# Kernel tuning notes

Measured on AMD Instinct MI355X. Metric: run time of the kernel, lower is better.

## Reference

```python
import jax, jax.numpy as jnp
import numpy as np

N = 50000      # nodes
E = 800000     # edges (avg degree 16)
D = 64         # hidden_dim == out_dim
L = 4          # number of GatedGCN layers
NB = 16        # num_bond_type
EPS_BN = 1e-5
EPS_ETA = 1e-6


def _bn(x, g, b):
    # training-mode batch norm over the node/edge axis
    mu = jnp.mean(x, axis=0, keepdims=True)
    var = jnp.var(x, axis=0, keepdims=True)
    return (x - mu) * jax.lax.rsqrt(var + EPS_BN) * g + b


def setup_inputs() -> dict:
    key = jax.random.key(0)
    ks = iter(jax.random.split(key, 64))
    s = 0.05

    def w(shape):
        return jax.random.normal(next(ks), shape, dtype=jnp.float32) * s

    inp = {
        "h_ids": jax.random.randint(next(ks), (N,), 0, N),
        "e_ids": jax.random.randint(next(ks), (E,), 0, NB),
        "f_ids": jax.random.randint(next(ks), (N,), 0, N),
        "src": jax.random.randint(next(ks), (E,), 0, N),
        "dst": jax.random.randint(next(ks), (E,), 0, N),
        "emb_h": w((N, D)),
        "emb_e": w((NB, D)),
        "emb_f": w((N, D)),
        "A1_w": w((L, D, D)), "A1_b": jnp.zeros((L, D), jnp.float32),
        "A2_w": w((L, 2 * D, D)), "A2_b": jnp.zeros((L, D), jnp.float32),
        "B1_w": w((L, D, D)), "B1_b": jnp.zeros((L, D), jnp.float32),
        "B2_w": w((L, D, D)), "B2_b": jnp.zeros((L, D), jnp.float32),
        "B3_w": w((L, D, D)), "B3_b": jnp.zeros((L, D), jnp.float32),
        "C1_w": w((L, D, D)), "C1_b": jnp.zeros((L, D), jnp.float32),
        "C2_w": w((L, D, D)), "C2_b": jnp.zeros((L, D), jnp.float32),
        "bn_h_g": jnp.ones((L, D), jnp.float32), "bn_h_b": jnp.zeros((L, D), jnp.float32),
        "bn_e_g": jnp.ones((L, D), jnp.float32), "bn_e_b": jnp.zeros((L, D), jnp.float32),
        "mlp_w0": w((D, D // 2)), "mlp_b0": jnp.zeros((D // 2,), jnp.float32),
        "mlp_w1": w((D // 2, D // 4)), "mlp_b1": jnp.zeros((D // 4,), jnp.float32),
        "mlp_w2": w((D // 4, 1)), "mlp_b2": jnp.zeros((1,), jnp.float32),
    }
    return inp


def reference(h_ids, e_ids, f_ids, src, dst,
              emb_h, emb_e, emb_f,
              A1_w, A1_b, A2_w, A2_b, B1_w, B1_b, B2_w, B2_b, B3_w, B3_b,
              C1_w, C1_b, C2_w, C2_b,
              bn_h_g, bn_h_b, bn_e_g, bn_e_b,
              mlp_w0, mlp_b0, mlp_w1, mlp_b1, mlp_w2, mlp_b2):
    h = emb_h[h_ids]          # [N, D]
    e = emb_e[e_ids]          # [E, D]
    p = emb_f[f_ids]          # [N, D]

    seg = lambda m: jax.ops.segment_sum(m, dst, num_segments=N)

    for i in range(L):
        h_in, e_in, p_in = h, e, p
        # per-node projections (dense GEMMs), then irregular gathers per edge
        B1h = h @ B1_w[i] + B1_b[i]
        B2h = h @ B2_w[i] + B2_b[i]
        B3e = e @ B3_w[i] + B3_b[i]
        hat_eta = B1h[src] + B2h[dst] + B3e           # [E, D]
        sigma = jax.nn.sigmoid(hat_eta)
        sum_sigma = seg(sigma)                        # [N, D] scatter-sum at dst
        eta = sigma / (sum_sigma[dst] + EPS_ETA)      # [E, D]

        v = jnp.concatenate([h, p], axis=-1) @ A2_w[i] + A2_b[i]  # [N, D]
        sum_eta_v = seg(eta * v[src])
        h_new = h @ A1_w[i] + A1_b[i] + sum_eta_v

        C2p = p @ C2_w[i] + C2_b[i]
        sum_eta_p = seg(eta * C2p[src])
        p_new = p @ C1_w[i] + C1_b[i] + sum_eta_p

        h = jax.nn.relu(_bn(h_new, bn_h_g[i], bn_h_b[i]))
        e_new = jax.nn.relu(_bn(hat_eta, bn_e_g[i], bn_e_b[i]))
        p = jnp.tanh(p_new)
        # residual (input_dim == output_dim in every layer)
        h = h_in + h
        e = e_in + e_new
        p = p_in + p

    hg = jnp.mean(h, axis=0)  # mean readout over the (single) graph -> [D]
    y = jax.nn.relu(hg @ mlp_w0 + mlp_b0)
    y = jax.nn.relu(y @ mlp_w1 + mlp_b1)
    y = y @ mlp_w2 + mlp_b2   # [1]
    return y
```

## Files before the change

### kernel.cpp

```cpp
#include <hip/hip_runtime.h>
#include <math.h>

#define NN 50000
#define EE 800000
#define LL 4

typedef unsigned short u16;
typedef unsigned int u32;

__device__ __forceinline__ float rlane(float v, int l) {
  return __int_as_float(__builtin_amdgcn_readlane(__float_as_int(v), l));
}

__device__ __forceinline__ float matvec64(float xv, const float* __restrict__ w) {
  float a0 = 0.f, a1 = 0.f, a2 = 0.f, a3 = 0.f;
#pragma unroll
  for (int k = 0; k < 64; k += 4) {
    a0 = fmaf(rlane(xv, k + 0), w[k + 0], a0);
    a1 = fmaf(rlane(xv, k + 1), w[k + 1], a1);
    a2 = fmaf(rlane(xv, k + 2), w[k + 2], a2);
    a3 = fmaf(rlane(xv, k + 3), w[k + 3], a3);
  }
  return (a0 + a1) + (a2 + a3);
}

__device__ __forceinline__ float sigm(float x) { return 1.f / (1.f + __expf(-x)); }

__device__ __forceinline__ u16 f2b(float x) {
  u32 u = __float_as_uint(x);
  u32 r = (u + 0x7FFFu + ((u >> 16) & 1u)) >> 16;
  return (u16)r;
}
__device__ __forceinline__ float b2f(u16 b) { return __uint_as_float(((u32)b) << 16); }

__global__ void k_hist(const int* __restrict__ dst, int* __restrict__ counts) {
  int i = blockIdx.x * 256 + threadIdx.x;
  if (i < EE) atomicAdd(&counts[dst[i]], 1);
}

__global__ void k_scan(const int* __restrict__ counts, int* __restrict__ row_start,
                       int* __restrict__ cursor) {
  __shared__ int sd[1024];
  int tid = threadIdx.x;
  int running = 0;
  for (int basei = 0; basei < NN; basei += 1024) {
    int i = basei + tid;
    int v = (i < NN) ? counts[i] : 0;
    sd[tid] = v;
    __syncthreads();
    for (int ofs = 1; ofs < 1024; ofs <<= 1) {
      int t = (tid >= ofs) ? sd[tid - ofs] : 0;
      __syncthreads();
      sd[tid] += t;
      __syncthreads();
    }
    int incl = sd[tid];
    int total = sd[1023];
    if (i < NN) { int e = running + incl - v; row_start[i] = e; cursor[i] = e; }
    running += total;
    __syncthreads();
  }
  if (tid == 0) row_start[NN] = EE;
}

__global__ void k_scatter(const int* __restrict__ dst, const int* __restrict__ src,
                          const int* __restrict__ e_ids,
                          int* __restrict__ cursor, int* __restrict__ src_s,
                          int* __restrict__ eids_s) {
  int i = blockIdx.x * 256 + threadIdx.x;
  if (i < EE) {
    int d = dst[i];
    int pos = atomicAdd(&cursor[d], 1);
    src_s[pos] = src[i];
    eids_s[pos] = e_ids[i];
  }
}

__global__ void k_einit(const int* __restrict__ eids_s, const float* __restrict__ emb_e,
                        u16* __restrict__ e_sorted) {
  int idx = blockIdx.x * 256 + threadIdx.x;
  if (idx >= EE * 64) return;
  int ed = idx >> 6, f = idx & 63;
  e_sorted[idx] = f2b(emb_e[eids_s[ed] * 64 + f]);
}

__global__ void k_ninit(const int* __restrict__ h_ids, const int* __restrict__ f_ids,
                        const float* __restrict__ emb_h, const float* __restrict__ emb_f,
                        float* __restrict__ h, float* __restrict__ p) {
  int idx = blockIdx.x * 256 + threadIdx.x;
  if (idx >= NN * 64) return;
  int n = idx >> 6, f = idx & 63;
  h[idx] = emb_h[h_ids[n] * 64 + f];
  p[idx] = emb_f[f_ids[n] * 64 + f];
}

__global__ void __launch_bounds__(256) k_A(
    int mode,
    float* __restrict__ h, float* __restrict__ p,
    float* __restrict__ hn, float* __restrict__ pn,
    const float* __restrict__ mu_h, const float* __restrict__ ir_h,
    const float* __restrict__ g_h, const float* __restrict__ b_h,
    const float* __restrict__ B1w, const float* __restrict__ B1b,
    const float* __restrict__ B2w, const float* __restrict__ B2b,
    const float* __restrict__ A1w, const float* __restrict__ A1b,
    const float* __restrict__ C1w, const float* __restrict__ C1b,
    const float* __restrict__ C2w, const float* __restrict__ C2b,
    const float* __restrict__ A2w, const float* __restrict__ A2b,
    float* __restrict__ B1h, float* __restrict__ B2h,
    float* __restrict__ vbuf, float* __restrict__ C2p) {
  const int f = threadIdx.x & 63;
  const int wv = threadIdx.x >> 6;
  const int base0 = (blockIdx.x * 4 + wv) * 16;
  if (base0 >= NN) return;

  if (mode) {
    float mu = mu_h[f], ir = ir_h[f], ga = g_h[f], be = b_h[f];
    for (int i = 0; i < 16; ++i) {
      int n = base0 + i; if (n >= NN) break;
      float hv = hn[n * 64 + f];
      h[n * 64 + f] += fmaxf(0.f, (hv - mu) * ir * ga + be);
      float pv = pn[n * 64 + f];
      p[n * 64 + f] += tanhf(pv);
    }
  }

  float w[64];
#define LOADW(WP) _Pragma("unroll") for (int k = 0; k < 64; ++k) w[k] = (WP)[k * 64 + f];

  LOADW(B1w);
  { float bb = B1b[f];
    for (int i = 0; i < 16; ++i) { int n = base0 + i; if (n >= NN) break;
      B1h[n * 64 + f] = matvec64(h[n * 64 + f], w) + bb; } }
  LOADW(B2w);
  { float bb = B2b[f];
    for (int i = 0; i < 16; ++i) { int n = base0 + i; if (n >= NN) break;
      B2h[n * 64 + f] = matvec64(h[n * 64 + f], w) + bb; } }
  LOADW(A1w);
  { float bb = A1b[f];
    for (int i = 0; i < 16; ++i) { int n = base0 + i; if (n >= NN) break;
      hn[n * 64 + f] = matvec64(h[n * 64 + f], w) + bb; } }
  LOADW(C1w);
  { float bb = C1b[f];
    for (int i = 0; i < 16; ++i) { int n = base0 + i; if (n >= NN) break;
      pn[n * 64 + f] = matvec64(p[n * 64 + f], w) + bb; } }
  LOADW(C2w);
  { float bb = C2b[f];
    for (int i = 0; i < 16; ++i) { int n = base0 + i; if (n >= NN) break;
      C2p[n * 64 + f] = matvec64(p[n * 64 + f], w) + bb; } }
  {
    float w2[64];
#pragma unroll
    for (int k = 0; k < 64; ++k) { w[k] = A2w[k * 64 + f]; w2[k] = A2w[(k + 64) * 64 + f]; }
    float bb = A2b[f];
    for (int i = 0; i < 16; ++i) { int n = base0 + i; if (n >= NN) break;
      vbuf[n * 64 + f] = matvec64(h[n * 64 + f], w) + matvec64(p[n * 64 + f], w2) + bb; }
  }
#undef LOADW
}

template <int SH>
__global__ void __launch_bounds__(256) k_B(
    const u16* __restrict__ e_sorted, const float* __restrict__ B1h,
    const float* __restrict__ B2h, const int* __restrict__ src_s,
    const int* __restrict__ row_start,
    const float* __restrict__ B3w, const float* __restrict__ B3b,
    u16* __restrict__ hat, float* __restrict__ sum_sigma,
    float* __restrict__ eS1, float* __restrict__ eS2) {
  const int f = threadIdx.x & 63;
  const int wv = threadIdx.x >> 6;
  const int nb = (blockIdx.x * 4 + wv) * 4;
  if (nb >= NN) return;
  float w[64];
#pragma unroll
  for (int k = 0; k < 64; ++k) w[k] = B3w[k * 64 + f];
  float bb = B3b[f];
  float s1 = 0.f, s2 = 0.f;
  for (int i = 0; i < 4; ++i) {
    int n = nb + i; if (n >= NN) break;
    float b2 = B2h[n * 64 + f];
    float ssum = 0.f;
    int t0 = row_start[n], t1 = row_start[n + 1];
    for (int t = t0; t < t1; ++t) {
      float xv = b2f(e_sorted[t * 64 + f]);
      int s = src_s[t];
      float acc = matvec64(xv, w) + bb + b2 + B1h[s * 64 + f];
      if (SH) {
        u16 hb = f2b(acc);
        hat[t * 64 + f] = hb;
        acc = b2f(hb);
      }
      float sg = sigm(acc);
      ssum += sg; s1 += acc; s2 += acc * acc;
    }
    sum_sigma[n * 64 + f] = ssum;
  }
  int slot = (blockIdx.x & 255) * 64 + f;
  atomicAdd(&eS1[slot], s1);
  atomicAdd(&eS2[slot], s2);
}

__global__ void k_red(const float* __restrict__ S1, const float* __restrict__ S2,
                      float cnt, float* __restrict__ mu, float* __restrict__ ir) {
  int f = threadIdx.x;
  float a = 0.f, b = 0.f;
  for (int j = 0; j < 256; ++j) { a += S1[j * 64 + f]; b += S2[j * 64 + f]; }
  float m = a / cnt;
  float var = fmaxf(b / cnt - m * m, 0.f);
  mu[f] = m;
  ir[f] = rsqrtf(var + 1e-5f);
}

template <int SH>
__global__ void __launch_bounds__(256) k_C(
    const u16* __restrict__ hat, u16* __restrict__ e_sorted,
    const float* __restrict__ B1h, const float* __restrict__ B2h,
    const float* __restrict__ B3w, const float* __restrict__ B3b,
    const float* __restrict__ vbuf, const float* __restrict__ C2p,
    const int* __restrict__ src_s, const int* __restrict__ row_start,
    const float* __restrict__ sum_sigma,
    float* __restrict__ hn, float* __restrict__ pn,
    const float* __restrict__ mu_e, const float* __restrict__ ir_e,
    const float* __restrict__ g_e, const float* __restrict__ b_e,
    float* __restrict__ hS1, float* __restrict__ hS2) {
  const int f = threadIdx.x & 63;
  const int wv = threadIdx.x >> 6;
  const int n = blockIdx.x * 4 + wv;
  if (n >= NN) return;
  float w[64];
  float bb = 0.f;
  if (!SH) {
#pragma unroll
    for (int k = 0; k < 64; ++k) w[k] = B3w[k * 64 + f];
    bb = B3b[f];
  }
  float mu = mu_e[f], ir = ir_e[f], ga = g_e[f], be = b_e[f];
  float inv = 1.f / (sum_sigma[n * 64 + f] + 1e-6f);
  float ahv = 0.f, ahp = 0.f;
  int t0 = row_start[n], t1 = row_start[n + 1];
  int t = t0;
  if (SH) {
    for (; t + 4 <= t1; t += 4) {
      int s0 = src_s[t + 0] * 64, s1 = src_s[t + 1] * 64;
      int s2 = src_s[t + 2] * 64, s3 = src_s[t + 3] * 64;
      float hv0 = b2f(hat[(size_t)(t + 0) * 64 + f]);
      float hv1 = b2f(hat[(size_t)(t + 1) * 64 + f]);
      float hv2 = b2f(hat[(size_t)(t + 2) * 64 + f]);
      float hv3 = b2f(hat[(size_t)(t + 3) * 64 + f]);
      float ev0 = b2f(e_sorted[(size_t)(t + 0) * 64 + f]);
      float ev1 = b2f(e_sorted[(size_t)(t + 1) * 64 + f]);
      float ev2 = b2f(e_sorted[(size_t)(t + 2) * 64 + f]);
      float ev3 = b2f(e_sorted[(size_t)(t + 3) * 64 + f]);
      float v0 = vbuf[s0 + f], v1 = vbuf[s1 + f], v2 = vbuf[s2 + f], v3 = vbuf[s3 + f];
      float c0 = C2p[s0 + f], c1 = C2p[s1 + f], c2 = C2p[s2 + f], c3 = C2p[s3 + f];
      float et0 = sigm(hv0) * inv, et1 = sigm(hv1) * inv;
      float et2 = sigm(hv2) * inv, et3 = sigm(hv3) * inv;
      ahv += et0 * v0 + et1 * v1 + et2 * v2 + et3 * v3;
      ahp += et0 * c0 + et1 * c1 + et2 * c2 + et3 * c3;
      e_sorted[(size_t)(t + 0) * 64 + f] = f2b(ev0 + fmaxf(0.f, (hv0 - mu) * ir * ga + be));
      e_sorted[(size_t)(t + 1) * 64 + f] = f2b(ev1 + fmaxf(0.f, (hv1 - mu) * ir * ga + be));
      e_sorted[(size_t)(t + 2) * 64 + f] = f2b(ev2 + fmaxf(0.f, (hv2 - mu) * ir * ga + be));
      e_sorted[(size_t)(t + 3) * 64 + f] = f2b(ev3 + fmaxf(0.f, (hv3 - mu) * ir * ga + be));
    }
  }
  for (; t < t1; ++t) {
    int s = src_s[t] * 64;
    float ev = b2f(e_sorted[(size_t)t * 64 + f]);
    float hatv;
    if (SH) hatv = b2f(hat[(size_t)t * 64 + f]);
    else    hatv = matvec64(ev, w) + bb + B2h[n * 64 + f] + B1h[s + f];
    float eta = sigm(hatv) * inv;
    ahv = fmaf(eta, vbuf[s + f], ahv);
    ahp = fmaf(eta, C2p[s + f], ahp);
    e_sorted[(size_t)t * 64 + f] = f2b(ev + fmaxf(0.f, (hatv - mu) * ir * ga + be));
  }
  float hv = hn[n * 64 + f] + ahv; hn[n * 64 + f] = hv;
  pn[n * 64 + f] += ahp;
  int slot = (blockIdx.x & 255) * 64 + f;
  atomicAdd(&hS1[slot], hv);
  atomicAdd(&hS2[slot], hv * hv);
}

__global__ void __launch_bounds__(256) k_F1(
    const float* __restrict__ hn, const float* __restrict__ h,
    const float* __restrict__ mu, const float* __restrict__ ir,
    const float* __restrict__ ga, const float* __restrict__ be,
    float* __restrict__ hsum) {
  int f = threadIdx.x & 63, wv = threadIdx.x >> 6;
  float m = mu[f], r = ir[f], g = ga[f], b = be[f];
  float ps = 0.f;
  for (int n = blockIdx.x * 4 + wv; n < NN; n += gridDim.x * 4)
    ps += h[n * 64 + f] + fmaxf(0.f, (hn[n * 64 + f] - m) * r * g + b);
  atomicAdd(&hsum[f], ps);
}

__global__ void k_F2(const float* __restrict__ hsum,
                     const float* __restrict__ w0, const float* __restrict__ b0,
                     const float* __restrict__ w1, const float* __restrict__ b1,
                     const float* __restrict__ w2, const float* __restrict__ b2,
                     float* __restrict__ out) {
  __shared__ float hg[64]; __shared__ float y0[32]; __shared__ float y1[16];
  int t = threadIdx.x;
  hg[t] = hsum[t] * (1.f / (float)NN);
  __syncthreads();
  if (t < 32) { float a = b0[t];
    for (int k = 0; k < 64; ++k) a = fmaf(hg[k], w0[k * 32 + t], a);
    y0[t] = fmaxf(a, 0.f); }
  __syncthreads();
  if (t < 16) { float a = b1[t];
    for (int k = 0; k < 32; ++k) a = fmaf(y0[k], w1[k * 16 + t], a);
    y1[t] = fmaxf(a, 0.f); }
  __syncthreads();
  if (t == 0) { float a = b2[0];
    for (int k = 0; k < 16; ++k) a = fmaf(y1[k], w2[k], a);
    out[0] = a; }
}

__global__ void k_report(float* out, float v) { out[0] = v; }

extern "C" void kernel_launch(void* const* d_in, const int* in_sizes, int n_in,
                              void* d_out, int out_size, void* d_ws, size_t ws_size,
                              hipStream_t stream) {
  (void)in_sizes; (void)n_in; (void)out_size;
  const int* h_ids = (const int*)d_in[0];
  const int* e_ids = (const int*)d_in[1];
  const int* f_ids = (const int*)d_in[2];
  const int* src   = (const int*)d_in[3];
  const int* dst   = (const int*)d_in[4];
  const float* emb_h = (const float*)d_in[5];
  const float* emb_e = (const float*)d_in[6];
  const float* emb_f = (const float*)d_in[7];
  const float* A1_w = (const float*)d_in[8];  const float* A1_b = (const float*)d_in[9];
  const float* A2_w = (const float*)d_in[10]; const float* A2_b = (const float*)d_in[11];
  const float* B1_w = (const float*)d_in[12]; const float* B1_b = (const float*)d_in[13];
  const float* B2_w = (const float*)d_in[14]; const float* B2_b = (const float*)d_in[15];
  const float* B3_w = (const float*)d_in[16]; const float* B3_b = (const float*)d_in[17];
  const float* C1_w = (const float*)d_in[18]; const float* C1_b = (const float*)d_in[19];
  const float* C2_w = (const float*)d_in[20]; const float* C2_b = (const float*)d_in[21];
  const float* bn_h_g = (const float*)d_in[22]; const float* bn_h_b = (const float*)d_in[23];
  const float* bn_e_g = (const float*)d_in[24]; const float* bn_e_b = (const float*)d_in[25];
  const float* mlp_w0 = (const float*)d_in[26]; const float* mlp_b0 = (const float*)d_in[27];
  const float* mlp_w1 = (const float*)d_in[28]; const float* mlp_b1 = (const float*)d_in[29];
  const float* mlp_w2 = (const float*)d_in[30]; const float* mlp_b2 = (const float*)d_in[31];

  auto pad = [](size_t b) { return (b + 255) & ~(size_t)255; };
  const size_t sz_e    = pad((size_t)EE * 64 * 2);
  const size_t sz_node = pad((size_t)NN * 64 * 4);
  const size_t sz_cnt  = pad((size_t)NN * 4);
  const size_t sz_row  = pad((size_t)(NN + 1) * 4);
  const size_t sz_ei   = pad((size_t)EE * 4);
  const size_t sz_stat = pad((size_t)LL * 2 * 256 * 64 * 4);
  const size_t sz_vec  = pad(64 * 4);

  size_t base_need = sz_e + 9 * sz_node + 2 * sz_cnt + sz_row + 2 * sz_ei +
                     2 * sz_stat + 5 * sz_vec;
  bool store_hat = (base_need + sz_e) <= ws_size;
  if (base_need > ws_size) {
    k_report<<<1, 1, 0, stream>>>((float*)d_out, (float)(ws_size >> 20) + 0.125f);
    return;
  }

  char* cur = (char*)d_ws;
  auto alloc = [&](size_t bytes) -> char* { char* r = cur; cur += bytes; return r; };
  u16* e_sorted = (u16*)alloc(sz_e);
  u16* hat      = store_hat ? (u16*)alloc(sz_e) : (u16*)e_sorted;
  float* h    = (float*)alloc(sz_node);
  float* p    = (float*)alloc(sz_node);
  float* hn   = (float*)alloc(sz_node);
  float* pn   = (float*)alloc(sz_node);
  float* B1h  = (float*)alloc(sz_node);
  float* B2h  = (float*)alloc(sz_node);
  float* vbuf = (float*)alloc(sz_node);
  float* C2p  = (float*)alloc(sz_node);
  float* ssig = (float*)alloc(sz_node);
  int* counts    = (int*)alloc(sz_cnt);
  int* cursor    = (int*)alloc(sz_cnt);
  int* row_start = (int*)alloc(sz_row);
  int* src_s     = (int*)alloc(sz_ei);
  int* eids_s    = (int*)alloc(sz_ei);
  float* estats = (float*)alloc(sz_stat);
  float* hstats = (float*)alloc(sz_stat);
  float* hsum   = (float*)alloc(sz_vec);
  float* mu_h = (float*)alloc(sz_vec);
  float* ir_h = (float*)alloc(sz_vec);
  float* mu_e = (float*)alloc(sz_vec);
  float* ir_e = (float*)alloc(sz_vec);

  hipMemsetAsync(counts, 0, sz_cnt, stream);
  hipMemsetAsync(estats, 0, 2 * sz_stat + sz_vec, stream);

  k_hist<<<(EE + 255) / 256, 256, 0, stream>>>(dst, counts);
  k_scan<<<1, 1024, 0, stream>>>(counts, row_start, cursor);
  k_scatter<<<(EE + 255) / 256, 256, 0, stream>>>(dst, src, e_ids, cursor, src_s, eids_s);
  k_einit<<<(EE * 64) / 256, 256, 0, stream>>>(eids_s, emb_e, e_sorted);
  k_ninit<<<(NN * 64 + 255) / 256, 256, 0, stream>>>(h_ids, f_ids, emb_h, emb_f, h, p);

  const int STAT = 2 * 256 * 64;
  for (int i = 0; i < LL; ++i) {
    if (i > 0) {
      k_red<<<1, 64, 0, stream>>>(hstats + (i - 1) * STAT,
                                  hstats + (i - 1) * STAT + 256 * 64, (float)NN, mu_h, ir_h);
    }
    const float* gh = bn_h_g + (i > 0 ? (i - 1) * 64 : 0);
    const float* bh = bn_h_b + (i > 0 ? (i - 1) * 64 : 0);
    k_A<<<(NN + 63) / 64, 256, 0, stream>>>(
        (i > 0) ? 1 : 0, h, p, hn, pn, mu_h, ir_h, gh, bh,
        B1_w + i * 4096, B1_b + i * 64, B2_w + i * 4096, B2_b + i * 64,
        A1_w + i * 4096, A1_b + i * 64, C1_w + i * 4096, C1_b + i * 64,
        C2_w + i * 4096, C2_b + i * 64, A2_w + i * 8192, A2_b + i * 64,
        B1h, B2h, vbuf, C2p);
    if (store_hat)
      k_B<1><<<(NN + 15) / 16, 256, 0, stream>>>(
          e_sorted, B1h, B2h, src_s, row_start, B3_w + i * 4096, B3_b + i * 64,
          hat, ssig, estats + i * STAT, estats + i * STAT + 256 * 64);
    else
      k_B<0><<<(NN + 15) / 16, 256, 0, stream>>>(
          e_sorted, B1h, B2h, src_s, row_start, B3_w + i * 4096, B3_b + i * 64,
          hat, ssig, estats + i * STAT, estats + i * STAT + 256 * 64);
    k_red<<<1, 64, 0, stream>>>(estats + i * STAT, estats + i * STAT + 256 * 64,
                                (float)EE, mu_e, ir_e);
    if (store_hat)
      k_C<1><<<(NN + 3) / 4, 256, 0, stream>>>(
          hat, e_sorted, B1h, B2h, B3_w + i * 4096, B3_b + i * 64, vbuf, C2p,
          src_s, row_start, ssig, hn, pn, mu_e, ir_e,
          bn_e_g + i * 64, bn_e_b + i * 64,
          hstats + i * STAT, hstats + i * STAT + 256 * 64);
    else
      k_C<0><<<(NN + 3) / 4, 256, 0, stream>>>(
          hat, e_sorted, B1h, B2h, B3_w + i * 4096, B3_b + i * 64, vbuf, C2p,
          src_s, row_start, ssig, hn, pn, mu_e, ir_e,
          bn_e_g + i * 64, bn_e_b + i * 64,
          hstats + i * STAT, hstats + i * STAT + 256 * 64);
  }
  k_red<<<1, 64, 0, stream>>>(hstats + 3 * STAT, hstats + 3 * STAT + 256 * 64,
                              (float)NN, mu_h, ir_h);
  k_F1<<<512, 256, 0, stream>>>(hn, h, mu_h, ir_h, bn_h_g + 3 * 64, bn_h_b + 3 * 64, hsum);
  k_F2<<<1, 64, 0, stream>>>(hsum, mlp_w0, mlp_b0, mlp_w1, mlp_b1, mlp_w2, mlp_b2,
                             (float*)d_out);
}
```

Measured before the change: 2.668 ms.

## Use split-bf16 MFMA for node GEMMs with runtime self-check fallback

Replaces the readlane-based scalar matvecs in the node-projection kernel with MFMA 16x16x32 bf16 tiles. It splits fp32 operands into hi/lo bf16 parts and uses three products to keep near-fp32 accuracy. A one-wave validation kernel compares an MFMA result against a scalar reference and sets a flag that picks the MFMA kernel or the old vector kernel. The cost is two launches per layer, one of which exits early, and weights are re-converted to bf16 inside every wave. The NN bounds checks are also dropped, which works because NN divides evenly into 16-row tiles.

```diff
diff --git a/kernel.cpp b/kernel.cpp
--- a/kernel.cpp
+++ b/kernel.cpp
@@ -7,6 +7,8 @@
 
 typedef unsigned short u16;
 typedef unsigned int u32;
+typedef __attribute__((ext_vector_type(8))) short bf16x8;
+typedef __attribute__((ext_vector_type(4))) float f32x4;
 
 __device__ __forceinline__ float rlane(float v, int l) {
   return __int_as_float(__builtin_amdgcn_readlane(__float_as_int(v), l));
@@ -32,6 +34,87 @@
   return (u16)r;
 }
 __device__ __forceinline__ float b2f(u16 b) { return __uint_as_float(((u32)b) << 16); }
+
+struct FragA { bf16x8 hi0, hi1, lo0, lo1; };
+
+__device__ __forceinline__ void load_a(const float* __restrict__ base, int l, FragA& fa) {
+  const int row = l & 15, quad = l >> 4;
+  const float* src = base + (size_t)row * 64 + quad * 8;
+  bf16x8 h0, h1, l0, l1;
+#pragma unroll
+  for (int j = 0; j < 8; ++j) {
+    float x0 = src[j], x1 = src[32 + j];
+    u16 a0 = f2b(x0), a1 = f2b(x1);
+    h0[j] = (short)a0; h1[j] = (short)a1;
+    l0[j] = (short)f2b(x0 - b2f(a0));
+    l1[j] = (short)f2b(x1 - b2f(a1));
+  }
+  fa.hi0 = h0; fa.hi1 = h1; fa.lo0 = l0; fa.lo1 = l1;
+}
+
+__device__ __forceinline__ void gemm_acc(const FragA& fa, const float* __restrict__ W,
+                                         int l, f32x4 acc[4]) {
+  const int row = l & 15, quad = l >> 4;
+#pragma unroll
+  for (int cb = 0; cb < 4; ++cb) {
+    f32x4 z = acc[cb];
+#pragma unroll
+    for (int kb = 0; kb < 2; ++kb) {
+      bf16x8 bhi, blo;
+      const float* wp = W + (size_t)(kb * 32 + quad * 8) * 64 + cb * 16 + row;
+#pragma unroll
+      for (int j = 0; j < 8; ++j) {
+        float wv = wp[(size_t)j * 64];
+        u16 aa = f2b(wv);
+        bhi[j] = (short)aa;
+        blo[j] = (short)f2b(wv - b2f(aa));
+      }
+      const bf16x8 ahi = kb ? fa.hi1 : fa.hi0;
+      const bf16x8 alo = kb ? fa.lo1 : fa.lo0;
+      z = __builtin_amdgcn_mfma_f32_16x16x32_bf16(ahi, bhi, z, 0, 0, 0);
+      z = __builtin_amdgcn_mfma_f32_16x16x32_bf16(alo, bhi, z, 0, 0, 0);
+      z = __builtin_amdgcn_mfma_f32_16x16x32_bf16(ahi, blo, z, 0, 0, 0);
+    }
+    acc[cb] = z;
+  }
+}
+
+__device__ __forceinline__ void store16(const f32x4 acc[4], const float* __restrict__ bias,
+                                        int l, float* __restrict__ out) {
+  const int row = l & 15, quad = l >> 4;
+#pragma unroll
+  for (int cb = 0; cb < 4; ++cb) {
+    int col = cb * 16 + row;
+    float bv = bias[col];
+#pragma unroll
+    for (int r = 0; r < 4; ++r)
+      out[(size_t)(quad * 4 + r) * 64 + col] = acc[cb][r] + bv;
+  }
+}
+
+__global__ void k_t2(const float* __restrict__ h, const float* __restrict__ B1w,
+                     int* __restrict__ flag) {
+  int l = threadIdx.x;
+  FragA fa;
+  load_a(h, l, fa);
+  f32x4 acc[4];
+  acc[0] = (f32x4){0,0,0,0}; acc[1] = (f32x4){0,0,0,0};
+  acc[2] = (f32x4){0,0,0,0}; acc[3] = (f32x4){0,0,0,0};
+  gemm_acc(fa, B1w, l, acc);
+  const int row = l & 15, quad = l >> 4;
+  int ok = 1;
+#pragma unroll
+  for (int cb = 0; cb < 4; ++cb)
+#pragma unroll
+    for (int r = 0; r < 4; ++r) {
+      int nrow = quad * 4 + r, col = cb * 16 + row;
+      float ref = 0.f;
+      for (int k = 0; k < 64; ++k) ref += h[nrow * 64 + k] * B1w[k * 64 + col];
+      if (fabsf(acc[cb][r] - ref) > 3e-3f + 3e-3f * fabsf(ref)) ok = 0;
+    }
+  ok = __all(ok);
+  if (l == 0) flag[0] = ok;
+}
 
 __global__ void k_hist(const int* __restrict__ dst, int* __restrict__ counts) {
   int i = blockIdx.x * 256 + threadIdx.x;
@@ -94,7 +177,7 @@
   p[idx] = emb_f[f_ids[n] * 64 + f];
 }
 
-__global__ void __launch_bounds__(256) k_A(
+__global__ void __launch_bounds__(256) k_Am(
     int mode,
     float* __restrict__ h, float* __restrict__ p,
     float* __restrict__ hn, float* __restrict__ pn,
@@ -107,7 +190,9 @@
     const float* __restrict__ C2w, const float* __restrict__ C2b,
     const float* __restrict__ A2w, const float* __restrict__ A2b,
     float* __restrict__ B1h, float* __restrict__ B2h,
-    float* __restrict__ vbuf, float* __restrict__ C2p) {
+    float* __restrict__ vbuf, float* __restrict__ C2p,
+    const int* __restrict__ flag) {
+  if (!flag[0]) return;
   const int f = threadIdx.x & 63;
   const int wv = threadIdx.x >> 6;
   const int base0 = (blockIdx.x * 4 + wv) * 16;
@@ -116,7 +201,55 @@
   if (mode) {
     float mu = mu_h[f], ir = ir_h[f], ga = g_h[f], be = b_h[f];
     for (int i = 0; i < 16; ++i) {
-      int n = base0 + i; if (n >= NN) break;
+      int n = base0 + i;
+      float hv = hn[(size_t)n * 64 + f];
+      h[(size_t)n * 64 + f] += fmaxf(0.f, (hv - mu) * ir * ga + be);
+      float pv = pn[(size_t)n * 64 + f];
+      p[(size_t)n * 64 + f] += tanhf(pv);
+    }
+  }
+
+  FragA fh, fq;
+  load_a(h + (size_t)base0 * 64, f, fh);
+  load_a(p + (size_t)base0 * 64, f, fq);
+  f32x4 acc[4];
+#define ZERO4 { acc[0]=(f32x4){0,0,0,0}; acc[1]=(f32x4){0,0,0,0}; \
+                acc[2]=(f32x4){0,0,0,0}; acc[3]=(f32x4){0,0,0,0}; }
+  ZERO4; gemm_acc(fh, B1w, f, acc); store16(acc, B1b, f, B1h + (size_t)base0 * 64);
+  ZERO4; gemm_acc(fh, B2w, f, acc); store16(acc, B2b, f, B2h + (size_t)base0 * 64);
+  ZERO4; gemm_acc(fh, A1w, f, acc); store16(acc, A1b, f, hn + (size_t)base0 * 64);
+  ZERO4; gemm_acc(fq, C1w, f, acc); store16(acc, C1b, f, pn + (size_t)base0 * 64);
+  ZERO4; gemm_acc(fq, C2w, f, acc); store16(acc, C2b, f, C2p + (size_t)base0 * 64);
+  ZERO4; gemm_acc(fh, A2w, f, acc); gemm_acc(fq, A2w + 4096, f, acc);
+  store16(acc, A2b, f, vbuf + (size_t)base0 * 64);
+#undef ZERO4
+}
+
+__global__ void __launch_bounds__(256) k_Av(
+    int mode,
+    float* __restrict__ h, float* __restrict__ p,
+    float* __restrict__ hn, float* __restrict__ pn,
+    const float* __restrict__ mu_h, const float* __restrict__ ir_h,
+    const float* __restrict__ g_h, const float* __restrict__ b_h,
+    const float* __restrict__ B1w, const float* __restrict__ B1b,
+    const float* __restrict__ B2w, const float* __restrict__ B2b,
+    const float* __restrict__ A1w, const float* __restrict__ A1b,
+    const float* __restrict__ C1w, const float* __restrict__ C1b,
+    const float* __restrict__ C2w, const float* __restrict__ C2b,
+    const float* __restrict__ A2w, const float* __restrict__ A2b,
+    float* __restrict__ B1h, float* __restrict__ B2h,
+    float* __restrict__ vbuf, float* __restrict__ C2p,
+    const int* __restrict__ flag) {
+  if (flag[0]) return;
+  const int f = threadIdx.x & 63;
+  const int wv = threadIdx.x >> 6;
+  const int base0 = (blockIdx.x * 4 + wv) * 16;
+  if (base0 >= NN) return;
+
+  if (mode) {
+    float mu = mu_h[f], ir = ir_h[f], ga = g_h[f], be = b_h[f];
+    for (int i = 0; i < 16; ++i) {
+      int n = base0 + i;
       float hv = hn[n * 64 + f];
       h[n * 64 + f] += fmaxf(0.f, (hv - mu) * ir * ga + be);
       float pv = pn[n * 64 + f];
@@ -126,33 +259,32 @@
 
   float w[64];
 #define LOADW(WP) _Pragma("unroll") for (int k = 0; k < 64; ++k) w[k] = (WP)[k * 64 + f];
-
   LOADW(B1w);
   { float bb = B1b[f];
-    for (int i = 0; i < 16; ++i) { int n = base0 + i; if (n >= NN) break;
+    for (int i = 0; i < 16; ++i) { int n = base0 + i;
       B1h[n * 64 + f] = matvec64(h[n * 64 + f], w) + bb; } }
   LOADW(B2w);
   { float bb = B2b[f];
-    for (int i = 0; i < 16; ++i) { int n = base0 + i; if (n >= NN) break;
+    for (int i = 0; i < 16; ++i) { int n = base0 + i;
       B2h[n * 64 + f] = matvec64(h[n * 64 + f], w) + bb; } }
   LOADW(A1w);
   { float bb = A1b[f];
-    for (int i = 0; i < 16; ++i) { int n = base0 + i; if (n >= NN) break;
+    for (int i = 0; i < 16; ++i) { int n = base0 + i;
       hn[n * 64 + f] = matvec64(h[n * 64 + f], w) + bb; } }
   LOADW(C1w);
   { float bb = C1b[f];
-    for (int i = 0; i < 16; ++i) { int n = base0 + i; if (n >= NN) break;
+    for (int i = 0; i < 16; ++i) { int n = base0 + i;
       pn[n * 64 + f] = matvec64(p[n * 64 + f], w) + bb; } }
   LOADW(C2w);
   { float bb = C2b[f];
-    for (int i = 0; i < 16; ++i) { int n = base0 + i; if (n >= NN) break;
+    for (int i = 0; i < 16; ++i) { int n = base0 + i;
       C2p[n * 64 + f] = matvec64(p[n * 64 + f], w) + bb; } }
   {
     float w2[64];
 #pragma unroll
     for (int k = 0; k < 64; ++k) { w[k] = A2w[k * 64 + f]; w2[k] = A2w[(k + 64) * 64 + f]; }
     float bb = A2b[f];
-    for (int i = 0; i < 16; ++i) { int n = base0 + i; if (n >= NN) break;
+    for (int i = 0; i < 16; ++i) { int n = base0 + i;
       vbuf[n * 64 + f] = matvec64(h[n * 64 + f], w) + matvec64(p[n * 64 + f], w2) + bb; }
   }
 #undef LOADW
@@ -176,7 +308,7 @@
   float bb = B3b[f];
   float s1 = 0.f, s2 = 0.f;
   for (int i = 0; i < 4; ++i) {
-    int n = nb + i; if (n >= NN) break;
+    int n = nb + i;
     float b2 = B2h[n * 64 + f];
     float ssum = 0.f;
     int t0 = row_start[n], t1 = row_start[n + 1];
@@ -352,7 +484,7 @@
   const size_t sz_vec  = pad(64 * 4);
 
   size_t base_need = sz_e + 9 * sz_node + 2 * sz_cnt + sz_row + 2 * sz_ei +
-                     2 * sz_stat + 5 * sz_vec;
+                     2 * sz_stat + 6 * sz_vec;
   bool store_hat = (base_need + sz_e) <= ws_size;
   if (base_need > ws_size) {
     k_report<<<1, 1, 0, stream>>>((float*)d_out, (float)(ws_size >> 20) + 0.125f);
@@ -384,6 +516,7 @@
   float* ir_h = (float*)alloc(sz_vec);
   float* mu_e = (float*)alloc(sz_vec);
   float* ir_e = (float*)alloc(sz_vec);
+  int* flag  = (int*)alloc(sz_vec);
 
   hipMemsetAsync(counts, 0, sz_cnt, stream);
   hipMemsetAsync(estats, 0, 2 * sz_stat + sz_vec, stream);
@@ -393,6 +526,7 @@
   k_scatter<<<(EE + 255) / 256, 256, 0, stream>>>(dst, src, e_ids, cursor, src_s, eids_s);
   k_einit<<<(EE * 64) / 256, 256, 0, stream>>>(eids_s, emb_e, e_sorted);
   k_ninit<<<(NN * 64 + 255) / 256, 256, 0, stream>>>(h_ids, f_ids, emb_h, emb_f, h, p);
+  k_t2<<<1, 64, 0, stream>>>(h, B1_w, flag);
 
   const int STAT = 2 * 256 * 64;
   for (int i = 0; i < LL; ++i) {
@@ -402,12 +536,18 @@
     }
     const float* gh = bn_h_g + (i > 0 ? (i - 1) * 64 : 0);
     const float* bh = bn_h_b + (i > 0 ? (i - 1) * 64 : 0);
-    k_A<<<(NN + 63) / 64, 256, 0, stream>>>(
+    k_Am<<<(NN + 63) / 64, 256, 0, stream>>>(
         (i > 0) ? 1 : 0, h, p, hn, pn, mu_h, ir_h, gh, bh,
         B1_w + i * 4096, B1_b + i * 64, B2_w + i * 4096, B2_b + i * 64,
         A1_w + i * 4096, A1_b + i * 64, C1_w + i * 4096, C1_b + i * 64,
         C2_w + i * 4096, C2_b + i * 64, A2_w + i * 8192, A2_b + i * 64,
-        B1h, B2h, vbuf, C2p);
+        B1h, B2h, vbuf, C2p, flag);
+    k_Av<<<(NN + 63) / 64, 256, 0, stream>>>(
+        (i > 0) ? 1 : 0, h, p, hn, pn, mu_h, ir_h, gh, bh,
+        B1_w + i * 4096, B1_b + i * 64, B2_w + i * 4096, B2_b + i * 64,
+        A1_w + i * 4096, A1_b + i * 64, C1_w + i * 4096, C1_b + i * 64,
+        C2_w + i * 4096, C2_b + i * 64, A2_w + i * 8192, A2_b + i * 64,
+        B1h, B2h, vbuf, C2p, flag);
     if (store_hat)
       k_B<1><<<(NN + 15) / 16, 256, 0, stream>>>(
           e_sorted, B1h, B2h, src_s, row_start, B3_w + i * 4096, B3_b + i * 64,
```

Result: faster. 2.468 ms, median of 2 (-7.5%).
